# Kernel optimization log

Measured on AMD Instinct MI355X. Metric: run time of the kernel, lower is better.

## Reference

```python
import jax, jax.numpy as jnp
import numpy as np

DIM = 1024
HEADS = 16
HEAD_DIM = DIM // HEADS
SCALE = DIM ** (-0.5)  # NOTE: module scales by full dim, not head dim


def setup_inputs() -> dict:
    key = jax.random.key(0)
    k1, k2, k3, k4 = jax.random.split(key, 4)
    x = jax.random.normal(k1, (4, 2048, DIM), dtype=jnp.float32)
    w_qkv = jax.random.normal(k2, (DIM, 3 * DIM), dtype=jnp.float32) * (DIM ** -0.5)
    w_out = jax.random.normal(k3, (DIM, DIM), dtype=jnp.float32) * (DIM ** -0.5)
    b_out = jax.random.normal(k4, (DIM,), dtype=jnp.float32) * 0.01
    return {"x": x, "w_qkv": w_qkv, "w_out": w_out, "b_out": b_out}


def reference(x, w_qkv, w_out, b_out):
    b, n, _ = x.shape
    qkv = x @ w_qkv  # [b, n, 3*dim]
    # 'b n (qkv h d) -> qkv b h n d'
    qkv = qkv.reshape(b, n, 3, HEADS, HEAD_DIM).transpose(2, 0, 3, 1, 4)
    q, k, v = qkv[0], qkv[1], qkv[2]  # each [b, h, n, d]
    dots = jnp.einsum('bhid,bhjd->bhij', q, k) * SCALE
    attn = jax.nn.softmax(dots, axis=-1)
    out = jnp.einsum('bhij,bhjd->bhid', attn, v)
    out = out.transpose(0, 2, 1, 3).reshape(b, n, DIM)  # 'b h n d -> b n (h d)'
    return out @ w_out + b_out
```

## Files before the change

### kernel.cpp

```cpp
#include <hip/hip_runtime.h>
#include <math.h>

#define BATCH 4
#define SEQ   2048
#define DMODEL 1024
#define HEADS 16
#define DHEAD 64
#define SCALE 0.03125f
#define KEXP  0.045084220027780106f
#define QKV_ELEMS (BATCH * HEADS * SEQ * DHEAD)

typedef __attribute__((ext_vector_type(8))) short short8;
typedef __attribute__((ext_vector_type(4))) float floatx4;
typedef unsigned int u32;

__device__ __forceinline__ unsigned short f2bf(float f) {
  union { float f; unsigned u; } v;
  v.f = f;
  return (unsigned short)((v.u + 0x7FFFu + ((v.u >> 16) & 1u)) >> 16);
}

__device__ __forceinline__ float fast_exp2(float x) {
#if __has_builtin(__builtin_amdgcn_exp2f)
  return __builtin_amdgcn_exp2f(x);
#else
  return __expf(x * 0.6931471805599453f);
#endif
}

__device__ __forceinline__ u32 pack_bf16(float p0, float p1) {
#if __has_builtin(__builtin_amdgcn_cvt_pk_bf16_f32)
  typedef __bf16 bf16x2 __attribute__((ext_vector_type(2)));
  bf16x2 t = __builtin_amdgcn_cvt_pk_bf16_f32(p0, p1);
  u32 r;
  __builtin_memcpy(&r, &t, 4);
  return r;
#else
  u32 a0 = __float_as_uint(p0) + 0x8000u;
  u32 a1 = __float_as_uint(p1) + 0x8000u;
  return __builtin_amdgcn_perm(a1, a0, 0x07060302);
#endif
}

__device__ __forceinline__ void async_ld16(const void* g, void* l) {
  __builtin_amdgcn_global_load_lds(
      (const __attribute__((address_space(1))) u32*)g,
      (__attribute__((address_space(3))) u32*)l, 16, 0, 0);
}

__device__ __forceinline__ void trans_tile(const float* __restrict__ W,
                                           unsigned short* __restrict__ WT,
                                           int K, int N, int n0, int k0,
                                           float (*tile)[33]) {
  const int tx = threadIdx.x & 31, ty = threadIdx.x >> 5;
#pragma unroll
  for (int i = 0; i < 4; ++i)
    tile[ty + i * 8][tx] = W[(size_t)(k0 + ty + i * 8) * N + n0 + tx];
  __syncthreads();
#pragma unroll
  for (int i = 0; i < 4; ++i)
    WT[(size_t)(n0 + ty + i * 8) * K + k0 + tx] = f2bf(tile[tx][ty + i * 8]);
}

__global__ __launch_bounds__(256) void prep_kernel(
    const float* __restrict__ x, const float* __restrict__ wqkv,
    const float* __restrict__ wout, unsigned short* __restrict__ xb,
    unsigned short* __restrict__ wqkvT, unsigned short* __restrict__ woutT) {
  __shared__ float tile[32][33];
  const int bx = blockIdx.x;
  if (bx < 8192) {
    size_t i = ((size_t)bx * 256 + threadIdx.x) * 4;
    float4 v = *(const float4*)(x + i);
    ushort4 o;
    o.x = f2bf(v.x); o.y = f2bf(v.y); o.z = f2bf(v.z); o.w = f2bf(v.w);
    *(ushort4*)(xb + i) = o;
  } else if (bx < 11264) {
    int t = bx - 8192;
    trans_tile(wqkv, wqkvT, 1024, 3072, (t % 96) * 32, (t / 96) * 32, tile);
  } else {
    int t = bx - 11264;
    trans_tile(wout, woutT, 1024, 1024, (t % 32) * 32, (t / 32) * 32, tile);
  }
}

__device__ __forceinline__ void gemm_core(
    const unsigned short* __restrict__ A, const unsigned short* __restrict__ BT,
    unsigned short* As, unsigned short* Bs, int m0, int n0,
    floatx4 acc[4][4]) {
  const int tid = threadIdx.x;
  const int wave = tid >> 6, lane = tid & 63;
  const int quad = lane >> 4, l16 = lane & 15;
  const int wm = wave >> 1, wn = wave & 1;
  const int lrow = lane >> 3, ls = lane & 7;
  const int dblk = ls ^ (lrow & 7);
  const int sw = l16 & 7;

#pragma unroll
  for (int mt = 0; mt < 4; ++mt)
#pragma unroll
    for (int nt = 0; nt < 4; ++nt) acc[mt][nt] = (floatx4){0.f, 0.f, 0.f, 0.f};

  for (int k0 = 0; k0 < DMODEL; k0 += 64) {
    __syncthreads();
#pragma unroll
    for (int i = 0; i < 4; ++i) {
      int chunk = wave * 4 + i;
      int row = chunk * 8 + lrow;
      async_ld16(A + (size_t)(m0 + row) * DMODEL + k0 + dblk * 8,
                 As + chunk * 512);
      async_ld16(BT + (size_t)(n0 + row) * DMODEL + k0 + dblk * 8,
                 Bs + chunk * 512);
    }
    __syncthreads();
#pragma unroll
    for (int kk = 0; kk < 64; kk += 32) {
      const int kb = kk >> 3;
      short8 a[4], b[4];
#pragma unroll
      for (int t = 0; t < 4; ++t) {
        int row = wm * 64 + t * 16 + l16;
        a[t] = *(short8*)(As + row * 64 + (((kb + quad) ^ sw) * 8));
        int rowb = wn * 64 + t * 16 + l16;
        b[t] = *(short8*)(Bs + rowb * 64 + (((kb + quad) ^ sw) * 8));
      }
#pragma unroll
      for (int mt = 0; mt < 4; ++mt)
#pragma unroll
        for (int nt = 0; nt < 4; ++nt)
          acc[mt][nt] = __builtin_amdgcn_mfma_f32_16x16x32_bf16(
              a[mt], b[nt], acc[mt][nt], 0, 0, 0);
    }
  }
}

__global__ __launch_bounds__(256) void gemm_qkv_kernel(
    const unsigned short* __restrict__ A, const unsigned short* __restrict__ BT,
    unsigned short* __restrict__ qk, unsigned short* __restrict__ vtg) {
  __shared__ __align__(16) unsigned char smem[128 * 136 * 2];
  unsigned short* As = (unsigned short*)smem;
  unsigned short* Bs = As + 128 * 64;
  unsigned short* T = (unsigned short*)smem;
  const int tid = threadIdx.x;
  const int wave = tid >> 6, lane = tid & 63;
  const int quad = lane >> 4, l16 = lane & 15;
  const int wm = wave >> 1, wn = wave & 1;
  const int m0 = blockIdx.y * 128, n0 = blockIdx.x * 128;
  floatx4 acc[4][4];
  gemm_core(A, BT, As, Bs, m0, n0, acc);

  const int b = m0 >> 11, ntok = m0 & 2047;
  __syncthreads();

  if (blockIdx.x < 16) {
    const float qsc = (blockIdx.x < 8) ? KEXP : 1.0f;
#pragma unroll
    for (int mt = 0; mt < 4; ++mt) {
#pragma unroll
      for (int nt = 0; nt < 4; ++nt) {
        int c = wn * 64 + nt * 16 + l16;
#pragma unroll
        for (int r = 0; r < 4; ++r) {
          int mloc = wm * 64 + mt * 16 + quad * 4 + r;
          T[mloc * 132 + c] = f2bf(acc[mt][nt][r] * qsc);
        }
      }
    }
    __syncthreads();
    const int which = blockIdx.x >> 3;
    const int h0 = (n0 >> 6) & 15;
    const int inner = tid & 7;
#pragma unroll
    for (int pass = 0; pass < 8; ++pass) {
      int row = pass * 32 + (tid >> 3);
      int token = row >> 1, hh = row & 1;
      *(short8*)(qk + (size_t)which * QKV_ELEMS +
                 (((size_t)((b * HEADS + h0 + hh) * SEQ + ntok + token)) << 6) +
                 inner * 8) = *(short8*)&T[token * 132 + hh * 64 + inner * 8];
    }
  } else {
#pragma unroll
    for (int mt = 0; mt < 4; ++mt) {
#pragma unroll
      for (int nt = 0; nt < 4; ++nt) {
        int c = wn * 64 + nt * 16 + l16;
#pragma unroll
        for (int r = 0; r < 4; ++r) {
          int mloc = wm * 64 + mt * 16 + quad * 4 + r;
          int pcm = (mloc & ~31) | ((mloc & 15) << 1) | ((mloc >> 4) & 1);
          T[c * 136 + pcm] = f2bf(acc[mt][nt][r]);
        }
      }
    }
    __syncthreads();
    const int c = tid >> 1, hh = tid & 1;
    const int nc = n0 - 2048 + c;
    const int h = nc >> 6, d = nc & 63;
    const size_t dstbase =
        (((size_t)(b * HEADS + h)) * DHEAD + d) * SEQ + ntok;
#pragma unroll
    for (int j = 0; j < 8; ++j) {
      int t0 = (2 * j + hh) * 8;
      *(short8*)(vtg + dstbase + t0) = *(short8*)&T[c * 136 + t0];
    }
  }
}

__global__ __launch_bounds__(256) void gemm_out_kernel(
    const unsigned short* __restrict__ A, const unsigned short* __restrict__ BT,
    const float* __restrict__ bias, float* __restrict__ C) {
  __shared__ __align__(16) unsigned short As[128 * 64];
  __shared__ __align__(16) unsigned short Bs[128 * 64];
  const int tid = threadIdx.x;
  const int wave = tid >> 6, lane = tid & 63;
  const int quad = lane >> 4, l16 = lane & 15;
  const int wm = wave >> 1, wn = wave & 1;
  const int m0 = blockIdx.y * 128, n0 = blockIdx.x * 128;
  floatx4 acc[4][4];
  gemm_core(A, BT, As, Bs, m0, n0, acc);

#pragma unroll
  for (int mt = 0; mt < 4; ++mt) {
#pragma unroll
    for (int nt = 0; nt < 4; ++nt) {
      int nc = n0 + wn * 64 + nt * 16 + l16;
      float bv = bias[nc];
#pragma unroll
      for (int r = 0; r < 4; ++r) {
        int m = m0 + wm * 64 + mt * 16 + quad * 4 + r;
        C[(size_t)m * DMODEL + nc] = acc[mt][nt][r] + bv;
      }
    }
  }
}

__global__ __launch_bounds__(256, 4) void attn_kernel(
    const unsigned short* __restrict__ Qb, const unsigned short* __restrict__ Kb,
    const unsigned short* __restrict__ Vtg, unsigned short* __restrict__ Op) {
  __shared__ __align__(16) unsigned short Ks[64 * 64];
  __shared__ __align__(16) unsigned short Vs[64 * 64];
  __shared__ __align__(16) unsigned short Pl[4][16][40];
  const int tid = threadIdx.x;
  const int wave = tid >> 6, lane = tid & 63;
  const int quad = lane >> 4, l16 = lane & 15;
  const int bh = blockIdx.x & 63, qt = blockIdx.x >> 6;
  const size_t base = (size_t)bh * SEQ * DHEAD;
  const int lrow = lane >> 3, ls = lane & 7;
  const int dblk = ls ^ (lrow & 7);
  const int sw = l16 & 7;

  short8 onesf;
#pragma unroll
  for (int i = 0; i < 8; ++i) onesf[i] = (short)0x3F80;

  short8 qf[2][2];
#pragma unroll
  for (int qs = 0; qs < 2; ++qs) {
    int qrow = qt * 128 + wave * 32 + qs * 16 + l16;
    qf[qs][0] = *(const short8*)(Qb + base + (size_t)qrow * DHEAD + quad * 8);
    qf[qs][1] =
        *(const short8*)(Qb + base + (size_t)qrow * DHEAD + 32 + quad * 8);
  }

  floatx4 o[2][4], lacc[2];
#pragma unroll
  for (int qs = 0; qs < 2; ++qs) {
    lacc[qs] = (floatx4){0.f, 0.f, 0.f, 0.f};
#pragma unroll
    for (int dt = 0; dt < 4; ++dt) o[qs][dt] = (floatx4){0.f, 0.f, 0.f, 0.f};
  }

  for (int kc = 0; kc < SEQ / 64; ++kc) {
    __syncthreads();
#pragma unroll
    for (int i = 0; i < 2; ++i) {
      int c = wave * 2 + i;
      int row = c * 8 + lrow;
      async_ld16(Kb + base + (size_t)(kc * 64 + row) * DHEAD + dblk * 8,
                 Ks + c * 512);
      async_ld16(Vtg + base + (size_t)row * SEQ + kc * 64 + dblk * 8,
                 Vs + c * 512);
    }
    __syncthreads();

#pragma unroll
    for (int kc2 = 0; kc2 < 2; ++kc2) {
      const int krow = kc2 * 32;
      short8 kf00 = *(short8*)(Ks + (krow + l16) * 64 + ((quad ^ sw) * 8));
      short8 kf01 = *(short8*)(Ks + (krow + l16) * 64 + (((4 + quad) ^ sw) * 8));
      short8 kf10 = *(short8*)(Ks + (krow + 16 + l16) * 64 + ((quad ^ sw) * 8));
      short8 kf11 =
          *(short8*)(Ks + (krow + 16 + l16) * 64 + (((4 + quad) ^ sw) * 8));
      short8 vf[4];
#pragma unroll
      for (int dt = 0; dt < 4; ++dt)
        vf[dt] = *(short8*)(Vs + (dt * 16 + l16) * 64 +
                            (((kc2 * 4 + quad) ^ sw) * 8));
#pragma unroll
      for (int qs = 0; qs < 2; ++qs) {
        floatx4 s0 = (floatx4){0.f, 0.f, 0.f, 0.f};
        floatx4 s1 = (floatx4){0.f, 0.f, 0.f, 0.f};
        s0 = __builtin_amdgcn_mfma_f32_16x16x32_bf16(qf[qs][0], kf00, s0, 0, 0, 0);
        s0 = __builtin_amdgcn_mfma_f32_16x16x32_bf16(qf[qs][1], kf01, s0, 0, 0, 0);
        s1 = __builtin_amdgcn_mfma_f32_16x16x32_bf16(qf[qs][0], kf10, s1, 0, 0, 0);
        s1 = __builtin_amdgcn_mfma_f32_16x16x32_bf16(qf[qs][1], kf11, s1, 0, 0, 0);
#pragma unroll
        for (int r = 0; r < 4; ++r) {
          float p0 = fast_exp2(s0[r]);
          float p1 = fast_exp2(s1[r]);
          *(u32*)&Pl[wave][quad * 4 + r][2 * l16] = pack_bf16(p0, p1);
        }
        short8 pf = *(short8*)&Pl[wave][l16][quad * 8];
        lacc[qs] =
            __builtin_amdgcn_mfma_f32_16x16x32_bf16(pf, onesf, lacc[qs], 0, 0, 0);
#pragma unroll
        for (int dt = 0; dt < 4; ++dt)
          o[qs][dt] = __builtin_amdgcn_mfma_f32_16x16x32_bf16(pf, vf[dt],
                                                              o[qs][dt], 0, 0, 0);
      }
    }
  }

  const int b = bh >> 4, h = bh & 15;
#pragma unroll
  for (int qs = 0; qs < 2; ++qs) {
#pragma unroll
    for (int r = 0; r < 4; ++r) {
      float inv = 1.f / lacc[qs][r];
      int n = qt * 128 + wave * 32 + qs * 16 + quad * 4 + r;
      size_t rowbase = ((size_t)(b * SEQ + n)) * DMODEL + h * DHEAD;
#pragma unroll
      for (int dt = 0; dt < 4; ++dt)
        Op[rowbase + dt * 16 + l16] = f2bf(o[qs][dt][r] * inv);
    }
  }
}

extern "C" void kernel_launch(void* const* d_in, const int* in_sizes, int n_in,
                              void* d_out, int out_size, void* d_ws,
                              size_t ws_size, hipStream_t stream) {
  const float* x = (const float*)d_in[0];
  const float* w_qkv = (const float*)d_in[1];
  const float* w_out = (const float*)d_in[2];
  const float* b_out = (const float*)d_in[3];
  float* out = (float*)d_out;

  unsigned short* ws = (unsigned short*)d_ws;
  unsigned short* xb = ws;
  unsigned short* wqkvT = xb + 8388608;
  unsigned short* woutT = wqkvT + 3145728;
  unsigned short* qb = woutT + 1048576;
  unsigned short* kb = qb + QKV_ELEMS;
  unsigned short* vtg = kb + QKV_ELEMS;
  unsigned short* op = vtg + QKV_ELEMS;

  prep_kernel<<<dim3(12288), dim3(256), 0, stream>>>(x, w_qkv, w_out, xb,
                                                     wqkvT, woutT);
  gemm_qkv_kernel<<<dim3(24, 64), dim3(256), 0, stream>>>(xb, wqkvT, qb, vtg);
  attn_kernel<<<dim3(1024), dim3(256), 0, stream>>>(qb, kb, vtg, op);
  gemm_out_kernel<<<dim3(8, 64), dim3(256), 0, stream>>>(op, woutT, b_out, out);
}
```

Measured before the change: 259.9 us.

## Double-buffer K/V tiles in LDS to overlap async loads with MFMA compute

The attention kernel now keeps two LDS buffers each for K and V. It issues the async global-to-LDS copy of the next 64-key chunk before computing on the current one, so each chunk needs one barrier instead of two. The aim is to hide global load latency behind the QK^T, exp and PV MFMA work instead of stalling on each tile. This roughly doubles the K/V LDS footprint, which could put pressure on the four-blocks-per-CU occupancy target.

```diff
diff --git a/kernel.cpp b/kernel.cpp
--- a/kernel.cpp
+++ b/kernel.cpp
@@ -236,8 +236,8 @@
 __global__ __launch_bounds__(256, 4) void attn_kernel(
     const unsigned short* __restrict__ Qb, const unsigned short* __restrict__ Kb,
     const unsigned short* __restrict__ Vtg, unsigned short* __restrict__ Op) {
-  __shared__ __align__(16) unsigned short Ks[64 * 64];
-  __shared__ __align__(16) unsigned short Vs[64 * 64];
+  __shared__ __align__(16) unsigned short Ks[2][64 * 64];
+  __shared__ __align__(16) unsigned short Vs[2][64 * 64];
   __shared__ __align__(16) unsigned short Pl[4][16][40];
   const int tid = threadIdx.x;
   const int wave = tid >> 6, lane = tid & 63;
@@ -248,6 +248,11 @@
   const int dblk = ls ^ (lrow & 7);
   const int sw = l16 & 7;
 
+  const unsigned short* kbase = Kb + base;
+  const unsigned short* vbase = Vtg + base;
+  const int c0 = wave * 2, c1 = wave * 2 + 1;
+  const int row0 = c0 * 8 + lrow, row1 = c1 * 8 + lrow;
+
   short8 onesf;
 #pragma unroll
   for (int i = 0; i < 8; ++i) onesf[i] = (short)0x3F80;
@@ -269,56 +274,71 @@
     for (int dt = 0; dt < 4; ++dt) o[qs][dt] = (floatx4){0.f, 0.f, 0.f, 0.f};
   }
 
-  for (int kc = 0; kc < SEQ / 64; ++kc) {
-    __syncthreads();
-#pragma unroll
-    for (int i = 0; i < 2; ++i) {
-      int c = wave * 2 + i;
-      int row = c * 8 + lrow;
-      async_ld16(Kb + base + (size_t)(kc * 64 + row) * DHEAD + dblk * 8,
-                 Ks + c * 512);
-      async_ld16(Vtg + base + (size_t)row * SEQ + kc * 64 + dblk * 8,
-                 Vs + c * 512);
-    }
-    __syncthreads();
-
-#pragma unroll
-    for (int kc2 = 0; kc2 < 2; ++kc2) {
-      const int krow = kc2 * 32;
-      short8 kf00 = *(short8*)(Ks + (krow + l16) * 64 + ((quad ^ sw) * 8));
-      short8 kf01 = *(short8*)(Ks + (krow + l16) * 64 + (((4 + quad) ^ sw) * 8));
-      short8 kf10 = *(short8*)(Ks + (krow + 16 + l16) * 64 + ((quad ^ sw) * 8));
-      short8 kf11 =
-          *(short8*)(Ks + (krow + 16 + l16) * 64 + (((4 + quad) ^ sw) * 8));
-      short8 vf[4];
-#pragma unroll
-      for (int dt = 0; dt < 4; ++dt)
-        vf[dt] = *(short8*)(Vs + (dt * 16 + l16) * 64 +
-                            (((kc2 * 4 + quad) ^ sw) * 8));
-#pragma unroll
-      for (int qs = 0; qs < 2; ++qs) {
-        floatx4 s0 = (floatx4){0.f, 0.f, 0.f, 0.f};
-        floatx4 s1 = (floatx4){0.f, 0.f, 0.f, 0.f};
-        s0 = __builtin_amdgcn_mfma_f32_16x16x32_bf16(qf[qs][0], kf00, s0, 0, 0, 0);
-        s0 = __builtin_amdgcn_mfma_f32_16x16x32_bf16(qf[qs][1], kf01, s0, 0, 0, 0);
-        s1 = __builtin_amdgcn_mfma_f32_16x16x32_bf16(qf[qs][0], kf10, s1, 0, 0, 0);
-        s1 = __builtin_amdgcn_mfma_f32_16x16x32_bf16(qf[qs][1], kf11, s1, 0, 0, 0);
-#pragma unroll
-        for (int r = 0; r < 4; ++r) {
-          float p0 = fast_exp2(s0[r]);
-          float p1 = fast_exp2(s1[r]);
-          *(u32*)&Pl[wave][quad * 4 + r][2 * l16] = pack_bf16(p0, p1);
-        }
-        short8 pf = *(short8*)&Pl[wave][l16][quad * 8];
-        lacc[qs] =
-            __builtin_amdgcn_mfma_f32_16x16x32_bf16(pf, onesf, lacc[qs], 0, 0, 0);
-#pragma unroll
-        for (int dt = 0; dt < 4; ++dt)
-          o[qs][dt] = __builtin_amdgcn_mfma_f32_16x16x32_bf16(pf, vf[dt],
-                                                              o[qs][dt], 0, 0, 0);
-      }
-    }
-  }
+#define STAGE(buf, kc)                                                         \
+  do {                                                                         \
+    async_ld16(kbase + (size_t)((kc)*64 + row0) * DHEAD + dblk * 8,            \
+               &Ks[buf][c0 * 512]);                                            \
+    async_ld16(vbase + (size_t)row0 * SEQ + (kc)*64 + dblk * 8,                \
+               &Vs[buf][c0 * 512]);                                            \
+    async_ld16(kbase + (size_t)((kc)*64 + row1) * DHEAD + dblk * 8,            \
+               &Ks[buf][c1 * 512]);                                            \
+    async_ld16(vbase + (size_t)row1 * SEQ + (kc)*64 + dblk * 8,                \
+               &Vs[buf][c1 * 512]);                                            \
+  } while (0)
+
+#define COMPUTE(buf)                                                           \
+  do {                                                                         \
+    _Pragma("unroll") for (int kc2 = 0; kc2 < 2; ++kc2) {                      \
+      const int krow = kc2 * 32;                                               \
+      short8 kf00 =                                                            \
+          *(short8*)(&Ks[buf][0] + (krow + l16) * 64 + ((quad ^ sw) * 8));     \
+      short8 kf01 = *(short8*)(&Ks[buf][0] + (krow + l16) * 64 +               \
+                               (((4 + quad) ^ sw) * 8));                       \
+      short8 kf10 = *(short8*)(&Ks[buf][0] + (krow + 16 + l16) * 64 +          \
+                               ((quad ^ sw) * 8));                             \
+      short8 kf11 = *(short8*)(&Ks[buf][0] + (krow + 16 + l16) * 64 +          \
+                               (((4 + quad) ^ sw) * 8));                       \
+      short8 vf[4];                                                            \
+      _Pragma("unroll") for (int dt = 0; dt < 4; ++dt) vf[dt] =                \
+          *(short8*)(&Vs[buf][0] + (dt * 16 + l16) * 64 +                      \
+                     (((kc2 * 4 + quad) ^ sw) * 8));                           \
+      _Pragma("unroll") for (int qs = 0; qs < 2; ++qs) {                       \
+        floatx4 s0 = (floatx4){0.f, 0.f, 0.f, 0.f};                            \
+        floatx4 s1 = (floatx4){0.f, 0.f, 0.f, 0.f};                            \
+        s0 = __builtin_amdgcn_mfma_f32_16x16x32_bf16(qf[qs][0], kf00, s0, 0,   \
+                                                     0, 0);                    \
+        s0 = __builtin_amdgcn_mfma_f32_16x16x32_bf16(qf[qs][1], kf01, s0, 0,   \
+                                                     0, 0);                    \
+        s1 = __builtin_amdgcn_mfma_f32_16x16x32_bf16(qf[qs][0], kf10, s1, 0,   \
+                                                     0, 0);                    \
+        s1 = __builtin_amdgcn_mfma_f32_16x16x32_bf16(qf[qs][1], kf11, s1, 0,   \
+                                                     0, 0);                    \
+        _Pragma("unroll") for (int r = 0; r < 4; ++r) {                        \
+          float p0 = fast_exp2(s0[r]);                                         \
+          float p1 = fast_exp2(s1[r]);                                         \
+          *(u32*)&Pl[wave][quad * 4 + r][2 * l16] = pack_bf16(p0, p1);         \
+        }                                                                      \
+        short8 pf = *(short8*)&Pl[wave][l16][quad * 8];                        \
+        lacc[qs] = __builtin_amdgcn_mfma_f32_16x16x32_bf16(pf, onesf,          \
+                                                           lacc[qs], 0, 0, 0); \
+        _Pragma("unroll") for (int dt = 0; dt < 4; ++dt) o[qs][dt] =           \
+            __builtin_amdgcn_mfma_f32_16x16x32_bf16(pf, vf[dt], o[qs][dt], 0,  \
+                                                    0, 0);                     \
+      }                                                                        \
+    }                                                                          \
+  } while (0)
+
+  STAGE(0, 0);
+  for (int kc = 0; kc < SEQ / 64; kc += 2) {
+    __syncthreads();
+    if (kc + 1 < SEQ / 64) STAGE(1, kc + 1);
+    COMPUTE(0);
+    __syncthreads();
+    if (kc + 2 < SEQ / 64) STAGE(0, kc + 2);
+    COMPUTE(1);
+  }
+#undef STAGE
+#undef COMPUTE
 
   const int b = bh >> 4, h = bh & 15;
 #pragma unroll
```

Result: no change. 259.2 us (-0.3%).
